# Kernel optimization log

Hardware: AMD Instinct MI355X
Metric: run time of the kernel (lower is better)

The kernel has to match this reference:

```python
import jax, jax.numpy as jnp
import numpy as np
from jax import lax

T, D, H, O = 16384, 257, 512, 257


def setup_inputs() -> dict:
    key = jax.random.key(0)
    ks = jax.random.split(key, 7)
    s = 1.0 / np.sqrt(H)  # PyTorch LSTM/Linear uniform init scale
    u = lambda k, shp: jax.random.uniform(k, shp, jnp.float32, -s, s)
    return {
        "stft": jax.random.normal(ks[0], (T, D), jnp.float32),
        "W_ih": u(ks[1], (4 * H, D)),
        "W_hh": u(ks[2], (4 * H, H)),
        "b_ih": u(ks[3], (4 * H,)),
        "b_hh": u(ks[4], (4 * H,)),
        "W_out": u(ks[5], (O, H)),
        "b_out": u(ks[6], (O,)),
    }


def reference(stft, W_ih, W_hh, b_ih, b_hh, W_out, b_out):
    # Batch size is 1 (stft.view(T, 1, -1)), so we scan over [T, D] directly.
    # Precompute input-to-gate GEMM for all timesteps: [T, 4H]
    x_gates = stft @ W_ih.T + (b_ih + b_hh)

    def step(carry, xg):
        h, c = carry  # [H], [H]
        g = xg + h @ W_hh.T  # [4H], PyTorch gate order: i, f, g, o
        i, f, gg, o = jnp.split(g, 4)
        i = jax.nn.sigmoid(i)
        f = jax.nn.sigmoid(f)
        gg = jnp.tanh(gg)
        o = jax.nn.sigmoid(o)
        c = f * c + i * gg
        h = o * jnp.tanh(c)
        return (h, c), h

    h0 = jnp.zeros((H,), stft.dtype)  # init_hidden(): zeros
    c0 = jnp.zeros((H,), stft.dtype)
    _, hs = lax.scan(step, (h0, c0), x_gates)  # hs: [T, H]

    out_space = hs @ W_out.T + b_out  # [T, O]
    return jax.nn.log_softmax(out_space, axis=1)
```

## Files before the change

kernel.cpp:

```cpp
#include <hip/hip_runtime.h>
#include <cmath>

#define T_STEPS 16384
#define D_IN    257
#define H_DIM   512
#define O_DIM   257
#define G4      2048

typedef unsigned long long u64;

#define WS_XG_OFF     8192
#define WS_HS_OFF     (8192 + (size_t)T_STEPS * G4 * 4)

__device__ inline float fast_sigmoid(float x) {
    return 1.f / (1.f + __expf(-x));
}
__device__ inline float fast_tanh(float x) {
    float ax = fminf(fabsf(x), 15.f);
    float e  = __expf(2.f * ax);
    float t  = (e - 1.f) / (e + 1.f);
    return copysignf(t, x);
}
__device__ inline float dot4(float4 a, float4 b) {
    return a.x * b.x + a.y * b.y + a.z * b.z + a.w * b.w;
}

#define PIN4(v) asm volatile("" : "+v"(v.x), "+v"(v.y), "+v"(v.z), "+v"(v.w))

#define AL(p) __hip_atomic_load((p), __ATOMIC_RELAXED, __HIP_MEMORY_SCOPE_AGENT)

__global__ __launch_bounds__(256) void xgate_gemm(
    const float* __restrict__ stft, const float* __restrict__ W_ih,
    const float* __restrict__ b_ih, const float* __restrict__ b_hh,
    float* __restrict__ xg)
{
    const int tid = threadIdx.x;
    const int tx = tid & 15, ty = tid >> 4;
    const int j0 = blockIdx.x * 128;
    const int t0 = blockIdx.y * 128;

    __shared__ float s_a[16][132];
    __shared__ float s_b[16][132];

    float acc[8][8] = {};

    for (int k0 = 0; k0 < D_IN; k0 += 16) {
        #pragma unroll
        for (int l = 0; l < 8; ++l) {
            int idx = tid + l * 256;
            int r   = idx >> 4;
            int kk  = idx & 15;
            int k   = k0 + kk;
            s_a[kk][r] = (k < D_IN) ? stft[(size_t)(t0 + r) * D_IN + k] : 0.f;
            s_b[kk][r] = (k < D_IN) ? W_ih[(size_t)(j0 + r) * D_IN + k] : 0.f;
        }
        __syncthreads();
        #pragma unroll
        for (int kk = 0; kk < 16; ++kk) {
            const float4* pa = (const float4*)&s_a[kk][ty * 8];
            const float4* pb = (const float4*)&s_b[kk][tx * 8];
            float4 a0 = pa[0], a1 = pa[1];
            float4 b0 = pb[0], b1 = pb[1];
            float ar[8] = {a0.x, a0.y, a0.z, a0.w, a1.x, a1.y, a1.z, a1.w};
            float br[8] = {b0.x, b0.y, b0.z, b0.w, b1.x, b1.y, b1.z, b1.w};
            #pragma unroll
            for (int r = 0; r < 8; ++r)
                #pragma unroll
                for (int c = 0; c < 8; ++c)
                    acc[r][c] += ar[r] * br[c];
        }
        __syncthreads();
    }

    float bias[8];
    #pragma unroll
    for (int c = 0; c < 8; ++c) {
        int j = j0 + tx * 8 + c;
        bias[c] = b_ih[j] + b_hh[j];
    }
    #pragma unroll
    for (int r = 0; r < 8; ++r) {
        int t = t0 + ty * 8 + r;
        #pragma unroll
        for (int c = 0; c < 8; ++c) {
            xg[(size_t)t * G4 + j0 + tx * 8 + c] = acc[r][c] + bias[c];
        }
    }
}

__global__ __launch_bounds__(512, 1) void lstm_seq(
    const float* __restrict__ W_hh, const float* __restrict__ xg,
    float* __restrict__ hs, u64* __restrict__ msg)
{
    const int tid  = threadIdx.x;
    const int g    = blockIdx.x;
    const int w    = tid >> 6;
    const int lane = tid & 63;
    const int j    = lane >> 2;
    const int c    = lane & 3;
    const int colb = w * 64 + c * 16;

    const float* wbase = W_hh + (size_t)(g * 16 + j) * H_DIM + colb;
    const size_t gstride = (size_t)H_DIM * H_DIM;
    float4 wA0, wA1, wA2, wA3, wB0, wB1, wB2, wB3;
    float4 wC0, wC1, wC2, wC3, wD0, wD1, wD2, wD3;
    {
        const float4* p0 = (const float4*)(wbase);
        const float4* p1 = (const float4*)(wbase + gstride);
        const float4* p2 = (const float4*)(wbase + 2 * gstride);
        const float4* p3 = (const float4*)(wbase + 3 * gstride);
        wA0 = p0[0]; wA1 = p0[1]; wA2 = p0[2]; wA3 = p0[3];
        wB0 = p1[0]; wB1 = p1[1]; wB2 = p1[2]; wB3 = p1[3];
        wC0 = p2[0]; wC1 = p2[1]; wC2 = p2[2]; wC3 = p2[3];
        wD0 = p3[0]; wD1 = p3[1]; wD2 = p3[2]; wD3 = p3[3];
    }
    PIN4(wA0); PIN4(wA1); PIN4(wA2); PIN4(wA3);
    PIN4(wB0); PIN4(wB1); PIN4(wB2); PIN4(wB3);
    PIN4(wC0); PIN4(wC1); PIN4(wC2); PIN4(wC3);
    PIN4(wD0); PIN4(wD1); PIN4(wD2); PIN4(wD3);

    __shared__ float s_h[512];
    __shared__ float s_part[2][512];

    u64* slot0 = msg;
    u64* slot1 = msg + 512;

    float c_state = 0.f;
    const int t_j = lane & 15;

    for (int t = 0; t < T_STEPS; ++t) {
        const unsigned tagt = (unsigned)t;
        const int buf = t & 1;

        float xv = 0.f;
        if (w == 0)
            xv = __builtin_nontemporal_load(
                xg + (size_t)t * G4 + (lane >> 4) * H_DIM + g * 16 + t_j);

        u64* rp = (buf ? slot1 : slot0) + tid;
        u64 u;
        {
            u64 p0 = AL(rp), p1 = AL(rp), p2 = AL(rp);
            for (;;) {
                u64 p3 = AL(rp);
                if ((unsigned)(p0 >> 32) == tagt) { u = p0; break; }
                p0 = AL(rp);
                if ((unsigned)(p1 >> 32) == tagt) { u = p1; break; }
                p1 = AL(rp);
                if ((unsigned)(p2 >> 32) == tagt) { u = p2; break; }
                p2 = AL(rp);
                if ((unsigned)(p3 >> 32) == tagt) { u = p3; break; }
            }
        }

        s_h[tid] = __uint_as_float((unsigned)u);

        const float4* hv = (const float4*)(s_h + colb);
        float4 h0 = hv[0], h1 = hv[1], h2 = hv[2], h3 = hv[3];

        float p0 = dot4(wA0, h0) + dot4(wA1, h1) + dot4(wA2, h2) + dot4(wA3, h3);
        float p1 = dot4(wB0, h0) + dot4(wB1, h1) + dot4(wB2, h2) + dot4(wB3, h3);
        float p2 = dot4(wC0, h0) + dot4(wC1, h1) + dot4(wC2, h2) + dot4(wC3, h3);
        float p3 = dot4(wD0, h0) + dot4(wD1, h1) + dot4(wD2, h2) + dot4(wD3, h3);

        const bool lo2 = (c < 2);
        float a0 = (lo2 ? p0 : p2) + __shfl_xor(lo2 ? p2 : p0, 2, 64);
        float a1 = (lo2 ? p1 : p3) + __shfl_xor(lo2 ? p3 : p1, 2, 64);
        const bool ev = ((c & 1) == 0);
        float fin = (ev ? a0 : a1) + __shfl_xor(ev ? a1 : a0, 1, 64);

        s_part[buf][w * 64 + c * 16 + j] = fin;

        asm volatile("s_waitcnt lgkmcnt(0)\n\ts_barrier" ::: "memory");

        if (w == 0) {
            const float* pp = &s_part[buf][0];
            float sum = xv;
            #pragma unroll
            for (int k = 0; k < 8; ++k) sum += pp[k * 64 + lane];

            float gi = __shfl(sum, t_j + 0,  64);
            float gf = __shfl(sum, t_j + 16, 64);
            float gg = __shfl(sum, t_j + 32, 64);
            float go = __shfl(sum, t_j + 48, 64);

            float iv = fast_sigmoid(gi);
            float fv = fast_sigmoid(gf);
            float ov = fast_sigmoid(go);
            float gv = fast_tanh(gg);
            c_state = fv * c_state + iv * gv;
            float hn = ov * fast_tanh(c_state);

            if (lane < 16) {
                u64 m = ((u64)(tagt + 1) << 32) | (u64)__float_as_uint(hn);
                u64* wp = (((t + 1) & 1) ? slot1 : slot0) + (g * 16 + lane);
                __hip_atomic_store(wp, m, __ATOMIC_RELAXED, __HIP_MEMORY_SCOPE_AGENT);
                __builtin_nontemporal_store(hn, hs + (size_t)t * H_DIM + g * 16 + lane);
            }
        }
    }
}

__global__ __launch_bounds__(256) void out_softmax(
    const float* __restrict__ hs, const float* __restrict__ W_out,
    const float* __restrict__ b_out, float* __restrict__ out)
{
    const int tid = threadIdx.x;
    const int t0  = blockIdx.x * 16;

    __shared__ float s_w[257 * 33];
    __shared__ float s_hs[16 * 33];
    __shared__ float s_o[16 * 257];
    __shared__ float s_red[8];

    float acc[16] = {};
    float acc256 = 0.f;

    for (int k0 = 0; k0 < H_DIM; k0 += 32) {
        for (int idx = tid; idx < 257 * 32; idx += 256) {
            int row = idx >> 5, col = idx & 31;
            s_w[row * 33 + col] = W_out[(size_t)row * H_DIM + k0 + col];
        }
        for (int idx = tid; idx < 16 * 32; idx += 256) {
            int row = idx >> 5, col = idx & 31;
            s_hs[row * 33 + col] = hs[(size_t)(t0 + row) * H_DIM + k0 + col];
        }
        __syncthreads();
        #pragma unroll
        for (int kk = 0; kk < 32; ++kk) {
            float w = s_w[tid * 33 + kk];
            #pragma unroll
            for (int r = 0; r < 16; ++r)
                acc[r] += s_hs[r * 33 + kk] * w;
        }
        if (tid < 16) {
            #pragma unroll
            for (int kk = 0; kk < 32; ++kk)
                acc256 += s_w[256 * 33 + kk] * s_hs[tid * 33 + kk];
        }
        __syncthreads();
    }

    float bias_c = b_out[tid];
    #pragma unroll
    for (int r = 0; r < 16; ++r) s_o[r * 257 + tid] = acc[r] + bias_c;
    if (tid < 16) s_o[tid * 257 + 256] = acc256 + b_out[256];
    __syncthreads();

    const int lane = tid & 63, wid = tid >> 6;
    for (int r = 0; r < 16; ++r) {
        float v  = s_o[r * 257 + tid];
        float vx = (tid == 0) ? s_o[r * 257 + 256] : -INFINITY;
        float m = fmaxf(v, vx);
        #pragma unroll
        for (int off = 32; off > 0; off >>= 1) m = fmaxf(m, __shfl_xor(m, off, 64));
        if (lane == 0) s_red[wid] = m;
        __syncthreads();
        m = fmaxf(fmaxf(s_red[0], s_red[1]), fmaxf(s_red[2], s_red[3]));
        float e = expf(v - m) + ((tid == 0) ? expf(vx - m) : 0.f);
        #pragma unroll
        for (int off = 32; off > 0; off >>= 1) e += __shfl_xor(e, off, 64);
        if (lane == 0) s_red[4 + wid] = e;
        __syncthreads();
        float s = s_red[4] + s_red[5] + s_red[6] + s_red[7];
        float lg = logf(s) + m;
        out[(size_t)(t0 + r) * O_DIM + tid] = v - lg;
        if (tid == 0) out[(size_t)(t0 + r) * O_DIM + 256] = vx - lg;
    }
}

extern "C" void kernel_launch(void* const* d_in, const int* in_sizes, int n_in,
                              void* d_out, int out_size, void* d_ws, size_t ws_size,
                              hipStream_t stream) {
    (void)in_sizes; (void)n_in; (void)out_size; (void)ws_size;

    const float* stft  = (const float*)d_in[0];
    const float* W_ih  = (const float*)d_in[1];
    const float* W_hh  = (const float*)d_in[2];
    const float* b_ih  = (const float*)d_in[3];
    const float* b_hh  = (const float*)d_in[4];
    const float* W_out = (const float*)d_in[5];
    const float* b_out = (const float*)d_in[6];
    float* out = (float*)d_out;

    char* ws = (char*)d_ws;
    u64* msg  = (u64*)ws;
    float* xg = (float*)(ws + WS_XG_OFF);
    float* hs = (float*)(ws + WS_HS_OFF);

    (void)hipMemsetAsync(ws, 0, 8192, stream);

    xgate_gemm<<<dim3(G4 / 128, T_STEPS / 128), 256, 0, stream>>>(
        stft, W_ih, b_ih, b_hh, xg);
    lstm_seq<<<32, 512, 0, stream>>>(W_hh, xg, hs, msg);
    out_softmax<<<T_STEPS / 16, 256, 0, stream>>>(hs, W_out, b_out, out);
}
```

Baseline: 28.41 ms.

## Split LSTM block into dedicated polling waves and compute waves with LDS flags

Doubles the recurrent kernel's block to 1024 threads. Eight extra waves do nothing but poll the cross-block h messages with hand-written pipelined inline-asm loads, write h into shared memory and raise a per-wave LDS flag. The compute waves spin on those flags instead of polling global memory themselves, and the gate activation is applied per-lane before the shuffle, so one activation runs per lane instead of four. This aims to take global polling latency off the compute waves' critical path, at the cost of more threads, a fragile s_barrier pairing between the two wave groups, and reliance on inline asm correctness.

```diff
diff --git a/kernel.cpp b/kernel.cpp
--- a/kernel.cpp
+++ b/kernel.cpp
@@ -26,8 +26,6 @@
 }
 
 #define PIN4(v) asm volatile("" : "+v"(v.x), "+v"(v.y), "+v"(v.z), "+v"(v.w))
-
-#define AL(p) __hip_atomic_load((p), __ATOMIC_RELAXED, __HIP_MEMORY_SCOPE_AGENT)
 
 __global__ __launch_bounds__(256) void xgate_gemm(
     const float* __restrict__ stft, const float* __restrict__ W_ih,
@@ -88,115 +86,161 @@
     }
 }
 
-__global__ __launch_bounds__(512, 1) void lstm_seq(
+__global__ __launch_bounds__(1024, 1) void lstm_seq(
     const float* __restrict__ W_hh, const float* __restrict__ xg,
     float* __restrict__ hs, u64* __restrict__ msg)
 {
     const int tid  = threadIdx.x;
     const int g    = blockIdx.x;
-    const int w    = tid >> 6;
-    const int lane = tid & 63;
-    const int j    = lane >> 2;
-    const int c    = lane & 3;
-    const int colb = w * 64 + c * 16;
-
-    const float* wbase = W_hh + (size_t)(g * 16 + j) * H_DIM + colb;
-    const size_t gstride = (size_t)H_DIM * H_DIM;
-    float4 wA0, wA1, wA2, wA3, wB0, wB1, wB2, wB3;
-    float4 wC0, wC1, wC2, wC3, wD0, wD1, wD2, wD3;
-    {
-        const float4* p0 = (const float4*)(wbase);
-        const float4* p1 = (const float4*)(wbase + gstride);
-        const float4* p2 = (const float4*)(wbase + 2 * gstride);
-        const float4* p3 = (const float4*)(wbase + 3 * gstride);
-        wA0 = p0[0]; wA1 = p0[1]; wA2 = p0[2]; wA3 = p0[3];
-        wB0 = p1[0]; wB1 = p1[1]; wB2 = p1[2]; wB3 = p1[3];
-        wC0 = p2[0]; wC1 = p2[1]; wC2 = p2[2]; wC3 = p2[3];
-        wD0 = p3[0]; wD1 = p3[1]; wD2 = p3[2]; wD3 = p3[3];
-    }
-    PIN4(wA0); PIN4(wA1); PIN4(wA2); PIN4(wA3);
-    PIN4(wB0); PIN4(wB1); PIN4(wB2); PIN4(wB3);
-    PIN4(wC0); PIN4(wC1); PIN4(wC2); PIN4(wC3);
-    PIN4(wD0); PIN4(wD1); PIN4(wD2); PIN4(wD3);
 
     __shared__ float s_h[512];
     __shared__ float s_part[2][512];
+    __shared__ int   s_flags[8];
 
     u64* slot0 = msg;
     u64* slot1 = msg + 512;
 
-    float c_state = 0.f;
-    const int t_j = lane & 15;
-
-    for (int t = 0; t < T_STEPS; ++t) {
-        const unsigned tagt = (unsigned)t;
-        const int buf = t & 1;
-
-        float xv = 0.f;
-        if (w == 0)
-            xv = __builtin_nontemporal_load(
-                xg + (size_t)t * G4 + (lane >> 4) * H_DIM + g * 16 + t_j);
-
-        u64* rp = (buf ? slot1 : slot0) + tid;
-        u64 u;
+    if (tid < 8) s_flags[tid] = -1;
+    __syncthreads();
+
+    if (tid < 512) {
+        const int w    = tid >> 6;
+        const int lane = tid & 63;
+        const int j    = lane >> 2;
+        const int c    = lane & 3;
+        const int colb = w * 64 + c * 16;
+
+        const float* wbase = W_hh + (size_t)(g * 16 + j) * H_DIM + colb;
+        const size_t gstride = (size_t)H_DIM * H_DIM;
+        float4 wA0, wA1, wA2, wA3, wB0, wB1, wB2, wB3;
+        float4 wC0, wC1, wC2, wC3, wD0, wD1, wD2, wD3;
         {
-            u64 p0 = AL(rp), p1 = AL(rp), p2 = AL(rp);
-            for (;;) {
-                u64 p3 = AL(rp);
-                if ((unsigned)(p0 >> 32) == tagt) { u = p0; break; }
-                p0 = AL(rp);
-                if ((unsigned)(p1 >> 32) == tagt) { u = p1; break; }
-                p1 = AL(rp);
-                if ((unsigned)(p2 >> 32) == tagt) { u = p2; break; }
-                p2 = AL(rp);
-                if ((unsigned)(p3 >> 32) == tagt) { u = p3; break; }
+            const float4* p0 = (const float4*)(wbase);
+            const float4* p1 = (const float4*)(wbase + gstride);
+            const float4* p2 = (const float4*)(wbase + 2 * gstride);
+            const float4* p3 = (const float4*)(wbase + 3 * gstride);
+            wA0 = p0[0]; wA1 = p0[1]; wA2 = p0[2]; wA3 = p0[3];
+            wB0 = p1[0]; wB1 = p1[1]; wB2 = p1[2]; wB3 = p1[3];
+            wC0 = p2[0]; wC1 = p2[1]; wC2 = p2[2]; wC3 = p2[3];
+            wD0 = p3[0]; wD1 = p3[1]; wD2 = p3[2]; wD3 = p3[3];
+        }
+        PIN4(wA0); PIN4(wA1); PIN4(wA2); PIN4(wA3);
+        PIN4(wB0); PIN4(wB1); PIN4(wB2); PIN4(wB3);
+        PIN4(wC0); PIN4(wC1); PIN4(wC2); PIN4(wC3);
+        PIN4(wD0); PIN4(wD1); PIN4(wD2); PIN4(wD3);
+
+        float c_state = 0.f;
+        const int t_j = lane & 15;
+        volatile int* fp = (volatile int*)&s_flags[w];
+
+        for (int t = 0; t < T_STEPS; ++t) {
+            const int buf = t & 1;
+
+            float xv = 0.f;
+            if (w == 0)
+                xv = __builtin_nontemporal_load(
+                    xg + (size_t)t * G4 + (lane >> 4) * H_DIM + g * 16 + t_j);
+
+            while (*fp != t) {}
+            asm volatile("" ::: "memory");
+
+            const float4* hv = (const float4*)(s_h + colb);
+            float4 h0 = hv[0], h1 = hv[1], h2 = hv[2], h3 = hv[3];
+
+            float p0 = dot4(wA0, h0) + dot4(wA1, h1) + dot4(wA2, h2) + dot4(wA3, h3);
+            float p1 = dot4(wB0, h0) + dot4(wB1, h1) + dot4(wB2, h2) + dot4(wB3, h3);
+            float p2 = dot4(wC0, h0) + dot4(wC1, h1) + dot4(wC2, h2) + dot4(wC3, h3);
+            float p3 = dot4(wD0, h0) + dot4(wD1, h1) + dot4(wD2, h2) + dot4(wD3, h3);
+
+            const bool lo2 = (c < 2);
+            float a0 = (lo2 ? p0 : p2) + __shfl_xor(lo2 ? p2 : p0, 2, 64);
+            float a1 = (lo2 ? p1 : p3) + __shfl_xor(lo2 ? p3 : p1, 2, 64);
+            const bool ev = ((c & 1) == 0);
+            float fin = (ev ? a0 : a1) + __shfl_xor(ev ? a1 : a0, 1, 64);
+
+            s_part[buf][w * 64 + c * 16 + j] = fin;
+
+            asm volatile("s_waitcnt lgkmcnt(0)\n\ts_barrier" ::: "memory");
+
+            if (w == 0) {
+                const float* pp = &s_part[buf][0];
+                float sum = xv;
+                #pragma unroll
+                for (int k = 0; k < 8; ++k) sum += pp[k * 64 + lane];
+
+                const int gate = lane >> 4;
+                float act = (gate == 2) ? fast_tanh(sum) : fast_sigmoid(sum);
+
+                float iv = __shfl(act, t_j + 0,  64);
+                float fv = __shfl(act, t_j + 16, 64);
+                float gv = __shfl(act, t_j + 32, 64);
+                float ov = __shfl(act, t_j + 48, 64);
+
+                c_state = fv * c_state + iv * gv;
+                float hn = ov * fast_tanh(c_state);
+
+                if (lane < 16) {
+                    u64 m = ((u64)(unsigned)(t + 1) << 32) | (u64)__float_as_uint(hn);
+                    u64* wp = (((t + 1) & 1) ? slot1 : slot0) + (g * 16 + lane);
+                    __hip_atomic_store(wp, m, __ATOMIC_RELAXED, __HIP_MEMORY_SCOPE_AGENT);
+                    __builtin_nontemporal_store(hn, hs + (size_t)t * H_DIM + g * 16 + lane);
+                }
             }
         }
-
-        s_h[tid] = __uint_as_float((unsigned)u);
-
-        const float4* hv = (const float4*)(s_h + colb);
-        float4 h0 = hv[0], h1 = hv[1], h2 = hv[2], h3 = hv[3];
-
-        float p0 = dot4(wA0, h0) + dot4(wA1, h1) + dot4(wA2, h2) + dot4(wA3, h3);
-        float p1 = dot4(wB0, h0) + dot4(wB1, h1) + dot4(wB2, h2) + dot4(wB3, h3);
-        float p2 = dot4(wC0, h0) + dot4(wC1, h1) + dot4(wC2, h2) + dot4(wC3, h3);
-        float p3 = dot4(wD0, h0) + dot4(wD1, h1) + dot4(wD2, h2) + dot4(wD3, h3);
-
-        const bool lo2 = (c < 2);
-        float a0 = (lo2 ? p0 : p2) + __shfl_xor(lo2 ? p2 : p0, 2, 64);
-        float a1 = (lo2 ? p1 : p3) + __shfl_xor(lo2 ? p3 : p1, 2, 64);
-        const bool ev = ((c & 1) == 0);
-        float fin = (ev ? a0 : a1) + __shfl_xor(ev ? a1 : a0, 1, 64);
-
-        s_part[buf][w * 64 + c * 16 + j] = fin;
-
-        asm volatile("s_waitcnt lgkmcnt(0)\n\ts_barrier" ::: "memory");
-
-        if (w == 0) {
-            const float* pp = &s_part[buf][0];
-            float sum = xv;
-            #pragma unroll
-            for (int k = 0; k < 8; ++k) sum += pp[k * 64 + lane];
-
-            float gi = __shfl(sum, t_j + 0,  64);
-            float gf = __shfl(sum, t_j + 16, 64);
-            float gg = __shfl(sum, t_j + 32, 64);
-            float go = __shfl(sum, t_j + 48, 64);
-
-            float iv = fast_sigmoid(gi);
-            float fv = fast_sigmoid(gf);
-            float ov = fast_sigmoid(go);
-            float gv = fast_tanh(gg);
-            c_state = fv * c_state + iv * gv;
-            float hn = ov * fast_tanh(c_state);
-
-            if (lane < 16) {
-                u64 m = ((u64)(tagt + 1) << 32) | (u64)__float_as_uint(hn);
-                u64* wp = (((t + 1) & 1) ? slot1 : slot0) + (g * 16 + lane);
-                __hip_atomic_store(wp, m, __ATOMIC_RELAXED, __HIP_MEMORY_SCOPE_AGENT);
-                __builtin_nontemporal_store(hn, hs + (size_t)t * H_DIM + g * 16 + lane);
-            }
+    } else {
+        const int widx = tid - 512;
+        const int m    = widx >> 6;
+        const int lane = widx & 63;
+
+        u64 s0 = 0, s1 = 0, s2 = 0, s3 = 0;
+
+        for (int t = 0; t < T_STEPS; ++t) {
+            u64* rp = ((t & 1) ? slot1 : slot0) + widx;
+            u64 addr = (u64)(uintptr_t)rp;
+            u64 th   = ((u64)(unsigned)t) << 32;
+            int k;
+
+            asm volatile(
+                "global_load_dwordx2 %[d0], %[ad], off sc0 sc1\n\t"
+                "global_load_dwordx2 %[d1], %[ad], off sc0 sc1\n\t"
+                "global_load_dwordx2 %[d2], %[ad], off sc0 sc1\n\t"
+                "global_load_dwordx2 %[d3], %[ad], off sc0 sc1\n\t"
+                "1:\n\t"
+                "s_waitcnt vmcnt(3)\n\t"
+                "v_cmp_lt_u64 vcc, %[d0], %[th]\n\t"
+                "s_cbranch_vccz 9f\n\t"
+                "global_load_dwordx2 %[d0], %[ad], off sc0 sc1\n\t"
+                "s_waitcnt vmcnt(3)\n\t"
+                "v_cmp_lt_u64 vcc, %[d1], %[th]\n\t"
+                "s_cbranch_vccz 8f\n\t"
+                "global_load_dwordx2 %[d1], %[ad], off sc0 sc1\n\t"
+                "s_waitcnt vmcnt(3)\n\t"
+                "v_cmp_lt_u64 vcc, %[d2], %[th]\n\t"
+                "s_cbranch_vccz 7f\n\t"
+                "global_load_dwordx2 %[d2], %[ad], off sc0 sc1\n\t"
+                "s_waitcnt vmcnt(3)\n\t"
+                "v_cmp_lt_u64 vcc, %[d3], %[th]\n\t"
+                "s_cbranch_vccz 6f\n\t"
+                "global_load_dwordx2 %[d3], %[ad], off sc0 sc1\n\t"
+                "s_branch 1b\n\t"
+                "6:\n\ts_mov_b32 %[k], 3\n\ts_branch 10f\n\t"
+                "7:\n\ts_mov_b32 %[k], 2\n\ts_branch 10f\n\t"
+                "8:\n\ts_mov_b32 %[k], 1\n\ts_branch 10f\n\t"
+                "9:\n\ts_mov_b32 %[k], 0\n\t"
+                "10:\n\t"
+                : [d0] "+v"(s0), [d1] "+v"(s1), [d2] "+v"(s2), [d3] "+v"(s3),
+                  [k] "=&s"(k)
+                : [ad] "v"(addr), [th] "s"(th)
+                : "vcc", "memory");
+
+            u64 u = (k == 0) ? s0 : (k == 1) ? s1 : (k == 2) ? s2 : s3;
+
+            s_h[widx] = __uint_as_float((unsigned)u);
+            asm volatile("s_waitcnt lgkmcnt(0)" ::: "memory");
+            if (lane == 0) *(volatile int*)&s_flags[m] = t;
+
+            asm volatile("s_barrier" ::: "memory");
+            asm volatile("" :: "v"(s0), "v"(s1), "v"(s2), "v"(s3));
         }
     }
 }
@@ -292,6 +336,6 @@
 
     xgate_gemm<<<dim3(G4 / 128, T_STEPS / 128), 256, 0, stream>>>(
         stft, W_ih, b_ih, b_hh, xg);
-    lstm_seq<<<32, 512, 0, stream>>>(W_hh, xg, hs, msg);
+    lstm_seq<<<32, 1024, 0, stream>>>(W_hh, xg, hs, msg);
     out_softmax<<<T_STEPS / 16, 256, 0, stream>>>(hs, W_out, b_out, out);
 }
```

Result: slower. 30.81 ms (+8.4%).

## Give each LSTM block a private mailbox and broadcast h writes per consumer

Applied to the files above, without the earlier changes.

Replaces the single shared h mailbox, which all 32 blocks polled, with a private mailbox copy per consumer block. Each producer wave now writes its new h values into all 32 block mailboxes, spreading the eight stores per lane across the wave. Polling is reduced to a simple single-load loop instead of the pipelined four-load loop. The aim is to cut contention on the same cache lines between readers and writers in the per-step cross-block sync. The cost is 32x more store traffic per step and a larger workspace region to zero.

```diff
diff --git a/kernel.cpp b/kernel.cpp
--- a/kernel.cpp
+++ b/kernel.cpp
@@ -6,11 +6,14 @@
 #define H_DIM   512
 #define O_DIM   257
 #define G4      2048
+#define NBLK    32
 
 typedef unsigned long long u64;
 
-#define WS_XG_OFF     8192
-#define WS_HS_OFF     (8192 + (size_t)T_STEPS * G4 * 4)
+#define WS_MSG_BYTES  (2 * NBLK * 512 * 8)
+#define WS_XG_OFF     WS_MSG_BYTES
+#define WS_HS_OFF     (WS_XG_OFF + (size_t)T_STEPS * G4 * 4)
+#define MBOX_BUF      (NBLK * 512)
 
 __device__ inline float fast_sigmoid(float x) {
     return 1.f / (1.f + __expf(-x));
@@ -26,8 +29,6 @@
 }
 
 #define PIN4(v) asm volatile("" : "+v"(v.x), "+v"(v.y), "+v"(v.z), "+v"(v.w))
-
-#define AL(p) __hip_atomic_load((p), __ATOMIC_RELAXED, __HIP_MEMORY_SCOPE_AGENT)
 
 __global__ __launch_bounds__(256) void xgate_gemm(
     const float* __restrict__ stft, const float* __restrict__ W_ih,
@@ -122,8 +123,8 @@
     __shared__ float s_h[512];
     __shared__ float s_part[2][512];
 
-    u64* slot0 = msg;
-    u64* slot1 = msg + 512;
+    u64* my0 = msg + (size_t)g * 512;
+    u64* my1 = msg + MBOX_BUF + (size_t)g * 512;
 
     float c_state = 0.f;
     const int t_j = lane & 15;
@@ -137,20 +138,11 @@
             xv = __builtin_nontemporal_load(
                 xg + (size_t)t * G4 + (lane >> 4) * H_DIM + g * 16 + t_j);
 
-        u64* rp = (buf ? slot1 : slot0) + tid;
+        u64* rp = (buf ? my1 : my0) + tid;
         u64 u;
-        {
-            u64 p0 = AL(rp), p1 = AL(rp), p2 = AL(rp);
-            for (;;) {
-                u64 p3 = AL(rp);
-                if ((unsigned)(p0 >> 32) == tagt) { u = p0; break; }
-                p0 = AL(rp);
-                if ((unsigned)(p1 >> 32) == tagt) { u = p1; break; }
-                p1 = AL(rp);
-                if ((unsigned)(p2 >> 32) == tagt) { u = p2; break; }
-                p2 = AL(rp);
-                if ((unsigned)(p3 >> 32) == tagt) { u = p3; break; }
-            }
+        for (;;) {
+            u = __hip_atomic_load(rp, __ATOMIC_RELAXED, __HIP_MEMORY_SCOPE_AGENT);
+            if ((unsigned)(u >> 32) == tagt) break;
         }
 
         s_h[tid] = __uint_as_float((unsigned)u);
@@ -191,10 +183,16 @@
             c_state = fv * c_state + iv * gv;
             float hn = ov * fast_tanh(c_state);
 
+            u64 m = ((u64)(tagt + 1) << 32) | (u64)__float_as_uint(hn);
+            u64* wb = msg + (((t + 1) & 1) ? MBOX_BUF : 0);
+            const int widx = g * 16 + t_j;
+            #pragma unroll
+            for (int k = 0; k < 8; ++k) {
+                int cdst = (lane >> 4) + 4 * k;
+                __hip_atomic_store(wb + (size_t)cdst * 512 + widx, m,
+                                   __ATOMIC_RELAXED, __HIP_MEMORY_SCOPE_AGENT);
+            }
             if (lane < 16) {
-                u64 m = ((u64)(tagt + 1) << 32) | (u64)__float_as_uint(hn);
-                u64* wp = (((t + 1) & 1) ? slot1 : slot0) + (g * 16 + lane);
-                __hip_atomic_store(wp, m, __ATOMIC_RELAXED, __HIP_MEMORY_SCOPE_AGENT);
                 __builtin_nontemporal_store(hn, hs + (size_t)t * H_DIM + g * 16 + lane);
             }
         }
@@ -288,10 +286,10 @@
     float* xg = (float*)(ws + WS_XG_OFF);
     float* hs = (float*)(ws + WS_HS_OFF);
 
-    (void)hipMemsetAsync(ws, 0, 8192, stream);
+    (void)hipMemsetAsync(ws, 0, WS_MSG_BYTES, stream);
 
     xgate_gemm<<<dim3(G4 / 128, T_STEPS / 128), 256, 0, stream>>>(
         stft, W_ih, b_ih, b_hh, xg);
-    lstm_seq<<<32, 512, 0, stream>>>(W_hh, xg, hs, msg);
+    lstm_seq<<<NBLK, 512, 0, stream>>>(W_hh, xg, hs, msg);
     out_softmax<<<T_STEPS / 16, 256, 0, stream>>>(hs, W_out, b_out, out);
 }
```

Measured after the change: 27.46 ms. 3.4% less time.
